# Kernel optimization log

Hardware: AMD Instinct MI355X
Metric: run time of the kernel (lower is better)

The kernel has to match this reference:

```python
import jax, jax.numpy as jnp
import numpy as np

EPS = 1e-09
MOMENTUM = 0.997
START_MOMENTUM = 0.8
WARMUP = 100

B, F, N = 32, 64, 128


def setup_inputs() -> dict:
    key = jax.random.key(0)
    k1, k2, k3 = jax.random.split(key, 3)
    return {
        "x": jax.random.normal(k1, (B, F, N, N), dtype=jnp.float32),
        "mask": jnp.ones((B, N), dtype=jnp.float32),
        "weight": jnp.ones((1, F, 1, 1), dtype=jnp.float32),
        "weight_exp": jax.random.normal(k2, (1, F, 1, 1), dtype=jnp.float32),
        "weight_bias": jnp.zeros((1, F, 1, 1), dtype=jnp.float32),
        "bias": jax.random.normal(k3, (1, F, 1), dtype=jnp.float32),
        "running_mean": jnp.zeros((F,), dtype=jnp.float32),
        "running_var": jnp.ones((F,), dtype=jnp.float32),
        "steps": 10,
    }


def reference(x, mask, weight, weight_exp, weight_bias, bias,
              running_mean, running_var, steps):
    # x: [B,F,N,N]; mask: [B,N]
    b, f, n, _ = x.shape
    eye = jnp.eye(n, dtype=x.dtype)
    # _reformat_mask -> [B,F,N,N]
    mask4 = mask[:, None, :, None] * mask[:, None, None, :]          # [B,1,N,N]
    mask4 = jnp.broadcast_to(mask4, x.shape)

    # _mean_and_variance_trace (training-mode batch statistics)
    num = jnp.einsum('bfii->bf', mask4)                              # node counts
    num2 = jnp.clip(num - 1.0, 1.0)
    x_sq = jnp.matmul(x, x)                                          # matrix_power(x, 2)
    trace = jnp.einsum('bfii,bfii->bf', x, mask4)
    trace_sq = jnp.einsum('bfii,bfii->bf', x_sq, mask4)
    mean = (trace / num).mean(axis=0)                                # [F]
    variance = (trace_sq / num2 - trace ** 2 / (num * num2)).mean(axis=0)

    # moving-average update with warmup (steps treated as static python int)
    if steps < WARMUP:
        beta = steps / WARMUP
        momentum = MOMENTUM * beta + START_MOMENTUM * (1.0 - beta)
    else:
        momentum = MOMENTUM
    rm = momentum * running_mean + (1.0 - momentum) * jax.lax.stop_gradient(mean)
    rv = momentum * running_var + (1.0 - momentum) * jax.lax.stop_gradient(variance)
    rm = jax.lax.stop_gradient(rm)
    rv = jax.lax.stop_gradient(rv)

    # subtract mean*I on the diagonal, normalize by sqrt(var), affine + diag bias
    m_t = rm[None, :, None, None] * eye                              # diag_embed -> [1,F,N,N]
    x_centered = (x - m_t) * mask4
    x_normalized = x_centered / (jnp.sqrt(rv)[None, :, None, None] + EPS)
    gain = weight * jnp.exp(weight_exp) + weight_bias                # [1,F,1,1]
    bias_t = bias[..., None] * eye                                   # [1,F,N,N]
    return x_normalized * gain + bias_t
```

## Files before the change

kernel.cpp:

```cpp
#include <hip/hip_runtime.h>

#define NB 32
#define NF 64
#define NN 128
#define EPSF 1e-9f

__global__ __launch_bounds__(256) void mfb_stats(
    const float* __restrict__ x, const float* __restrict__ mask,
    float* __restrict__ mean_bf, float* __restrict__ var_bf) {
  __shared__ float tile[NN * NN];
  const int tid = threadIdx.x;
  const int bf = blockIdx.x;
  const int b = bf >> 6;
  const float* xp = x + (size_t)bf * (NN * NN);
  const int lane = tid & 63;

  float m0 = mask[b * NN + lane];
  float m1 = mask[b * NN + 64 + lane];
  float msq0 = m0 * m0;
  float msq1 = m1 * m1;

  const int kcol = tid & 127;
  const int ib = tid >> 7;
#pragma unroll 8
  for (int c = 0; c < 64; ++c) {
    int i = 2 * c + ib;
    tile[i * NN + (kcol ^ (i & 31))] = xp[c * 256 + tid];
  }
  __syncthreads();

  float tr = 0.f, nump = 0.f;
  if (tid < 64) nump = msq0 + msq1;
  if (tid < 128) {
    float d = tile[tid * NN + (tid ^ (tid & 31))];
    tr = d * ((tid < 64) ? msq0 : msq1);
  }

  const int irow = tid >> 1;
  const int k0 = (tid & 1) << 6;
  float mq = (irow < 64) ? __shfl(msq0, irow, 64) : __shfl(msq1, irow - 64, 64);
  const int cxor = irow & 31;
  const int rowbase = irow * NN;
  float acc = 0.f;
#pragma unroll
  for (int c = 0; c < 64; ++c) {
    int k = k0 + c;
    float a = tile[rowbase + (k ^ cxor)];
    float bt = tile[k * NN + (irow ^ (k & 31))];
    acc = fmaf(a, bt, acc);
  }
  float trsq = acc * mq;

#pragma unroll
  for (int off = 32; off > 0; off >>= 1) {
    tr   += __shfl_down(tr, off, 64);
    trsq += __shfl_down(trsq, off, 64);
    nump += __shfl_down(nump, off, 64);
  }
  __syncthreads();
  if (lane == 0) {
    int w = tid >> 6;
    tile[w * 3 + 0] = tr;
    tile[w * 3 + 1] = trsq;
    tile[w * 3 + 2] = nump;
  }
  __syncthreads();
  if (tid == 0) {
    float trs = tile[0] + tile[3] + tile[6] + tile[9];
    float tq  = tile[1] + tile[4] + tile[7] + tile[10];
    float num = tile[2] + tile[5] + tile[8] + tile[11];
    float num2 = fmaxf(num - 1.f, 1.f);
    mean_bf[bf] = trs / num;
    var_bf[bf]  = tq / num2 - trs * trs / (num * num2);
  }
}

__global__ void mfb_finalize(
    const float* __restrict__ mean_bf, const float* __restrict__ var_bf,
    const float* __restrict__ w, const float* __restrict__ wexp,
    const float* __restrict__ wbias, const float* __restrict__ rmean,
    const float* __restrict__ rvar, const int* __restrict__ steps,
    float* __restrict__ rmA, float* __restrict__ sA) {
  int f = threadIdx.x;
  float ms = 0.f, vs = 0.f;
  for (int b = 0; b < NB; ++b) {
    ms += mean_bf[b * NF + f];
    vs += var_bf[b * NF + f];
  }
  ms *= (1.f / NB);
  vs *= (1.f / NB);
  int st = steps[0];
  float mom = 0.997f;
  if (st < 100) {
    float beta = (float)st * 0.01f;
    mom = 0.997f * beta + 0.8f * (1.f - beta);
  }
  float rm = mom * rmean[f] + (1.f - mom) * ms;
  float rv = mom * rvar[f] + (1.f - mom) * vs;
  float gain = w[f] * expf(wexp[f]) + wbias[f];
  rmA[f] = rm;
  sA[f] = gain / (sqrtf(rv) + EPSF);
}

__global__ __launch_bounds__(256) void mfb_apply(
    const float4* __restrict__ x4, const float* __restrict__ mask,
    const float* __restrict__ rmA, const float* __restrict__ sA,
    const float* __restrict__ bias, float4* __restrict__ out4) {
  const int total = NB * NF * NN * NN / 4;
  for (int v = blockIdx.x * 256 + threadIdx.x; v < total;
       v += gridDim.x * 256) {
    float4 xv = x4[v];
    int j0 = (v & 31) << 2;
    int i = (v >> 5) & 127;
    int f = (v >> 12) & 63;
    int b = v >> 18;
    float4 mj = ((const float4*)(mask + b * NN))[v & 31];
    float mi = mask[b * NN + i];
    float s = sA[f];
    float rm = rmA[f];
    float bi = bias[f];
    float cs = mi * s;
    float4 o;
    o.x = (xv.x - ((i == j0    ) ? rm : 0.f)) * (cs * mj.x) + ((i == j0    ) ? bi : 0.f);
    o.y = (xv.y - ((i == j0 + 1) ? rm : 0.f)) * (cs * mj.y) + ((i == j0 + 1) ? bi : 0.f);
    o.z = (xv.z - ((i == j0 + 2) ? rm : 0.f)) * (cs * mj.z) + ((i == j0 + 2) ? bi : 0.f);
    o.w = (xv.w - ((i == j0 + 3) ? rm : 0.f)) * (cs * mj.w) + ((i == j0 + 3) ? bi : 0.f);
    out4[v] = o;
  }
}

extern "C" void kernel_launch(void* const* d_in, const int* in_sizes, int n_in,
                              void* d_out, int out_size, void* d_ws, size_t ws_size,
                              hipStream_t stream) {
  const float* x     = (const float*)d_in[0];
  const float* mask  = (const float*)d_in[1];
  const float* w     = (const float*)d_in[2];
  const float* wexp  = (const float*)d_in[3];
  const float* wbias = (const float*)d_in[4];
  const float* bias  = (const float*)d_in[5];
  const float* rmean = (const float*)d_in[6];
  const float* rvar  = (const float*)d_in[7];
  const int*   steps = (const int*)d_in[8];

  float* ws = (float*)d_ws;
  float* mean_bf = ws;
  float* var_bf  = ws + NB * NF;
  float* rmA     = ws + 2 * NB * NF;
  float* sA      = rmA + NF;

  mfb_stats<<<NB * NF, 256, 0, stream>>>(x, mask, mean_bf, var_bf);
  mfb_finalize<<<1, NF, 0, stream>>>(mean_bf, var_bf, w, wexp, wbias,
                                     rmean, rvar, steps, rmA, sA);
  mfb_apply<<<2048, 256, 0, stream>>>((const float4*)x, mask, rmA, sA, bias,
                                      (float4*)d_out);
}
```

Measured before the change: 74.82 us.

## Fuse finalize into apply kernel with per-(b,f) blocks and nontemporal stores

```diff
diff --git a/kernel.cpp b/kernel.cpp
--- a/kernel.cpp
+++ b/kernel.cpp
@@ -4,6 +4,8 @@
 #define NF 64
 #define NN 128
 #define EPSF 1e-9f
+
+typedef float f32x4 __attribute__((ext_vector_type(4)));
 
 __global__ __launch_bounds__(256) void mfb_stats(
     const float* __restrict__ x, const float* __restrict__ mask,
@@ -75,57 +77,69 @@
   }
 }
 
-__global__ void mfb_finalize(
+__global__ __launch_bounds__(256) void mfb_apply(
+    const f32x4* __restrict__ x4, const float* __restrict__ mask,
     const float* __restrict__ mean_bf, const float* __restrict__ var_bf,
     const float* __restrict__ w, const float* __restrict__ wexp,
-    const float* __restrict__ wbias, const float* __restrict__ rmean,
-    const float* __restrict__ rvar, const int* __restrict__ steps,
-    float* __restrict__ rmA, float* __restrict__ sA) {
-  int f = threadIdx.x;
-  float ms = 0.f, vs = 0.f;
-  for (int b = 0; b < NB; ++b) {
-    ms += mean_bf[b * NF + f];
-    vs += var_bf[b * NF + f];
+    const float* __restrict__ wbias, const float* __restrict__ bias,
+    const float* __restrict__ rmean, const float* __restrict__ rvar,
+    const int* __restrict__ steps, f32x4* __restrict__ out4) {
+  const int bf = blockIdx.x;
+  const int b = bf >> 6;
+  const int f = bf & 63;
+  const int tid = threadIdx.x;
+  __shared__ float smask[NN];
+  __shared__ float sc[3];
+
+  if (tid < NN) smask[tid] = mask[b * NN + tid];
+  if (tid < 32) {
+    float ms = mean_bf[tid * NF + f];
+    float vs = var_bf[tid * NF + f];
+#pragma unroll
+    for (int off = 16; off > 0; off >>= 1) {
+      ms += __shfl_down(ms, off, 32);
+      vs += __shfl_down(vs, off, 32);
+    }
+    if (tid == 0) {
+      ms *= (1.f / NB);
+      vs *= (1.f / NB);
+      int st = steps[0];
+      float mom = 0.997f;
+      if (st < 100) {
+        float beta = (float)st * 0.01f;
+        mom = 0.997f * beta + 0.8f * (1.f - beta);
+      }
+      float rm = mom * rmean[f] + (1.f - mom) * ms;
+      float rv = mom * rvar[f] + (1.f - mom) * vs;
+      float gain = w[f] * expf(wexp[f]) + wbias[f];
+      sc[0] = rm;
+      sc[1] = gain / (sqrtf(rv) + EPSF);
+      sc[2] = bias[f];
+    }
   }
-  ms *= (1.f / NB);
-  vs *= (1.f / NB);
-  int st = steps[0];
-  float mom = 0.997f;
-  if (st < 100) {
-    float beta = (float)st * 0.01f;
-    mom = 0.997f * beta + 0.8f * (1.f - beta);
-  }
-  float rm = mom * rmean[f] + (1.f - mom) * ms;
-  float rv = mom * rvar[f] + (1.f - mom) * vs;
-  float gain = w[f] * expf(wexp[f]) + wbias[f];
-  rmA[f] = rm;
-  sA[f] = gain / (sqrtf(rv) + EPSF);
-}
+  __syncthreads();
 
-__global__ __launch_bounds__(256) void mfb_apply(
-    const float4* __restrict__ x4, const float* __restrict__ mask,
-    const float* __restrict__ rmA, const float* __restrict__ sA,
-    const float* __restrict__ bias, float4* __restrict__ out4) {
-  const int total = NB * NF * NN * NN / 4;
-  for (int v = blockIdx.x * 256 + threadIdx.x; v < total;
-       v += gridDim.x * 256) {
-    float4 xv = x4[v];
-    int j0 = (v & 31) << 2;
-    int i = (v >> 5) & 127;
-    int f = (v >> 12) & 63;
-    int b = v >> 18;
-    float4 mj = ((const float4*)(mask + b * NN))[v & 31];
-    float mi = mask[b * NN + i];
-    float s = sA[f];
-    float rm = rmA[f];
-    float bi = bias[f];
-    float cs = mi * s;
-    float4 o;
-    o.x = (xv.x - ((i == j0    ) ? rm : 0.f)) * (cs * mj.x) + ((i == j0    ) ? bi : 0.f);
-    o.y = (xv.y - ((i == j0 + 1) ? rm : 0.f)) * (cs * mj.y) + ((i == j0 + 1) ? bi : 0.f);
-    o.z = (xv.z - ((i == j0 + 2) ? rm : 0.f)) * (cs * mj.z) + ((i == j0 + 2) ? bi : 0.f);
-    o.w = (xv.w - ((i == j0 + 3) ? rm : 0.f)) * (cs * mj.w) + ((i == j0 + 3) ? bi : 0.f);
-    out4[v] = o;
+  const float rm = sc[0];
+  const float s = sc[1];
+  const float bi = sc[2];
+  const f32x4 mj4 = ((const f32x4*)smask)[tid & 31];
+  const int j0 = (tid & 31) << 2;
+  const int wv = tid >> 5;
+  const f32x4* xp = x4 + (size_t)bf * 4096;
+  f32x4* op = out4 + (size_t)bf * 4096;
+
+#pragma unroll
+  for (int c = 0; c < 16; ++c) {
+    const int idx = c * 256 + tid;
+    const int i = c * 8 + wv;
+    f32x4 xv = xp[idx];
+    float cs = smask[i] * s;
+    f32x4 o;
+    o.x = (xv.x - ((i == j0    ) ? rm : 0.f)) * (cs * mj4.x) + ((i == j0    ) ? bi : 0.f);
+    o.y = (xv.y - ((i == j0 + 1) ? rm : 0.f)) * (cs * mj4.y) + ((i == j0 + 1) ? bi : 0.f);
+    o.z = (xv.z - ((i == j0 + 2) ? rm : 0.f)) * (cs * mj4.z) + ((i == j0 + 2) ? bi : 0.f);
+    o.w = (xv.w - ((i == j0 + 3) ? rm : 0.f)) * (cs * mj4.w) + ((i == j0 + 3) ? bi : 0.f);
+    __builtin_nontemporal_store(o, &op[idx]);
   }
 }
 
@@ -145,12 +159,9 @@
   float* ws = (float*)d_ws;
   float* mean_bf = ws;
   float* var_bf  = ws + NB * NF;
-  float* rmA     = ws + 2 * NB * NF;
-  float* sA      = rmA + NF;
 
   mfb_stats<<<NB * NF, 256, 0, stream>>>(x, mask, mean_bf, var_bf);
-  mfb_finalize<<<1, NF, 0, stream>>>(mean_bf, var_bf, w, wexp, wbias,
-                                     rmean, rvar, steps, rmA, sA);
-  mfb_apply<<<2048, 256, 0, stream>>>((const float4*)x, mask, rmA, sA, bias,
-                                      (float4*)d_out);
+  mfb_apply<<<NB * NF, 256, 0, stream>>>((const f32x4*)x, mask, mean_bf, var_bf,
+                                         w, wexp, wbias, bias, rmean, rvar,
+                                         steps, (f32x4*)d_out);
 }
```

Measured after the change: 72.60 us. 3.0% less time.
